# Optimization experiments

Hardware: AMD Instinct MI355X
Metric: run time of the kernel (lower is better)

Reference implementation:

```python
import jax, jax.numpy as jnp
import numpy as np

B, S, D, F, E, K = 2, 1024, 2048, 1024, 8, 2


def setup_inputs() -> dict:
    key = jax.random.key(0)
    ks = jax.random.split(key, 5)
    scale_x = 0.02
    return {
        "x": jax.random.normal(ks[0], (B, S, D), dtype=jnp.float32),
        "w_router": jax.random.normal(ks[1], (E, D), dtype=jnp.float32) * scale_x,
        "w_gate": jax.random.normal(ks[2], (E, F, D), dtype=jnp.float32) * scale_x,
        "w_up": jax.random.normal(ks[3], (E, F, D), dtype=jnp.float32) * scale_x,
        "w_down": jax.random.normal(ks[4], (E, D, F), dtype=jnp.float32) * scale_x,
        "top_k": K,
    }


def reference(x, w_router, w_gate, w_up, w_down, top_k):
    # Router: logits [B,S,E] -> top-k indices + softmax over top-k logits (fp32)
    logits = jnp.einsum("bsd,ed->bse", x, w_router)
    top_logits, top_idx = jax.lax.top_k(logits, top_k)          # [B,S,K]
    gates = jax.nn.softmax(top_logits.astype(jnp.float32), axis=-1)
    # SwitchGLU: per-expert gated MLP. Compute all experts densely, then gather
    # the selected expert output per token (reference-faithful math).
    h = jax.nn.silu(jnp.einsum("bsd,efd->besf", x, w_gate)) * jnp.einsum(
        "bsd,efd->besf", x, w_up
    )                                                            # [B,E,S,F]
    out_all = jnp.einsum("besf,edf->bsed", h, w_down)            # [B,S,E,D]
    y = jnp.take_along_axis(out_all, top_idx[..., None], axis=2)  # [B,S,K,D]
    return (y * gates[..., None].astype(y.dtype)).sum(axis=-2)   # [B,S,D]
```

## Files before the change

kernel.cpp:

```cpp
#include <hip/hip_runtime.h>
#include <hip/hip_bf16.h>

#define T_TOK 2048
#define DIM   2048
#define FFN   1024
#define NE    8

typedef __attribute__((ext_vector_type(8))) short bf16x8;
typedef __attribute__((ext_vector_type(4))) float f32x4;

__device__ __forceinline__ unsigned short f2bf(float f) {
  __hip_bfloat16 h = __float2bfloat16(f);
  return __builtin_bit_cast(unsigned short, h);
}

__device__ __forceinline__ void gload_lds16(const unsigned short* g, unsigned short* l) {
  __builtin_amdgcn_global_load_lds(
      (const __attribute__((address_space(1))) void*)g,
      (__attribute__((address_space(3))) void*)l, 16, 0, 0);
}

__global__ void zero_out(float4* __restrict__ o, int n4) {
  int i = blockIdx.x * blockDim.x + threadIdx.x;
  int stride = gridDim.x * blockDim.x;
  float4 z = {0.f, 0.f, 0.f, 0.f};
  for (; i < n4; i += stride) o[i] = z;
}

__global__ __launch_bounds__(256) void cvt_w(
    const float* __restrict__ wg, const float* __restrict__ wu, const float* __restrict__ wd,
    unsigned short* __restrict__ wgb, unsigned short* __restrict__ wub,
    unsigned short* __restrict__ wdb) {
  int b = blockIdx.x;
  const float* src; unsigned short* dst;
  if (b < 2048)       { src = wg; dst = wgb; }
  else if (b < 4096)  { src = wu; dst = wub; b -= 2048; }
  else                { src = wd; dst = wdb; b -= 4096; }
  const f32x4* s = reinterpret_cast<const f32x4*>(src) + (long)b * 2048 + threadIdx.x;
  ushort4* d = reinterpret_cast<ushort4*>(dst) + (long)b * 2048 + threadIdx.x;
  f32x4 v[8];
#pragma unroll
  for (int g = 0; g < 8; ++g) v[g] = __builtin_nontemporal_load(&s[g * 256]);
#pragma unroll
  for (int g = 0; g < 8; ++g) {
    ushort4 o;
    o.x = f2bf(v[g][0]); o.y = f2bf(v[g][1]); o.z = f2bf(v[g][2]); o.w = f2bf(v[g][3]);
    d[g * 256] = o;
  }
}

__global__ __launch_bounds__(256) void router_topk(
    const float* __restrict__ x, const float* __restrict__ wr,
    int* __restrict__ top_i, float* __restrict__ top_g,
    unsigned short* __restrict__ xb) {
  int t = blockIdx.x * 4 + (threadIdx.x >> 6);
  int lane = threadIdx.x & 63;
  const float4* xr = reinterpret_cast<const float4*>(x) + (size_t)t * (DIM / 4);
  const float4* wrv = reinterpret_cast<const float4*>(wr);
  ushort4* xbr = reinterpret_cast<ushort4*>(xb + (size_t)t * DIM);
  float acc[NE];
#pragma unroll
  for (int e = 0; e < NE; ++e) acc[e] = 0.f;
#pragma unroll
  for (int it = 0; it < DIM / 4 / 64; ++it) {
    int d4 = it * 64 + lane;
    float4 xv = xr[d4];
    ushort4 o;
    o.x = f2bf(xv.x); o.y = f2bf(xv.y); o.z = f2bf(xv.z); o.w = f2bf(xv.w);
    xbr[d4] = o;
#pragma unroll
    for (int e = 0; e < NE; ++e) {
      float4 wv = wrv[e * (DIM / 4) + d4];
      acc[e] += xv.x * wv.x + xv.y * wv.y + xv.z * wv.z + xv.w * wv.w;
    }
  }
#pragma unroll
  for (int off = 32; off > 0; off >>= 1) {
#pragma unroll
    for (int e = 0; e < NE; ++e) acc[e] += __shfl_xor(acc[e], off, 64);
  }
  if (lane == 0) {
    int i0 = 0; float m0 = acc[0];
#pragma unroll
    for (int e = 1; e < NE; ++e) if (acc[e] > m0) { m0 = acc[e]; i0 = e; }
    int i1 = -1; float m1 = -3.4e38f;
#pragma unroll
    for (int e = 0; e < NE; ++e) if (e != i0 && acc[e] > m1) { m1 = acc[e]; i1 = e; }
    float tv = expf(m1 - m0);
    float den = 1.f + tv;
    top_i[t * 2 + 0] = i0; top_i[t * 2 + 1] = i1;
    top_g[t * 2 + 0] = 1.f / den; top_g[t * 2 + 1] = tv / den;
  }
}

__global__ void count_offsets(const int* __restrict__ top_i,
                              int* __restrict__ offs, int* __restrict__ cursor) {
  __shared__ int cnt[NE];
  if (threadIdx.x < NE) cnt[threadIdx.x] = 0;
  __syncthreads();
  for (int i = threadIdx.x; i < T_TOK * 2; i += blockDim.x) atomicAdd(&cnt[top_i[i]], 1);
  __syncthreads();
  if (threadIdx.x == 0) {
    int s = 0;
    for (int e = 0; e < NE; ++e) { offs[e] = s; cursor[e] = s; s += cnt[e]; }
    offs[NE] = s;
  }
}

__global__ void scatter_tokens(const int* __restrict__ top_i, const float* __restrict__ top_g,
                               int* __restrict__ cursor, int* __restrict__ tok_list,
                               float* __restrict__ gate_lst) {
  int t = blockIdx.x * blockDim.x + threadIdx.x;
  if (t >= T_TOK) return;
#pragma unroll
  for (int s = 0; s < 2; ++s) {
    int e = top_i[t * 2 + s];
    int p = atomicAdd(&cursor[e], 1);
    tok_list[p] = t;
    gate_lst[p] = top_g[t * 2 + s];
  }
}

__global__ __launch_bounds__(256, 4) void gateup_gemm(
    const unsigned short* __restrict__ xb, const unsigned short* __restrict__ wgb,
    const unsigned short* __restrict__ wub, const int* __restrict__ tok_list,
    const int* __restrict__ offs, unsigned short* __restrict__ hbuf) {
  const int e = blockIdx.z;
  const int row0 = offs[e];
  const int n_e = offs[e + 1] - row0;
  const int mt = blockIdx.y;
  if (mt * 64 >= n_e) return;
  const int nt = blockIdx.x;

  __shared__ unsigned short As[64 * 64];
  __shared__ unsigned short Bg[64 * 64];
  __shared__ unsigned short Bu[64 * 64];

  const int tid = threadIdx.x;
  const int wid = tid >> 6;
  const int lane = tid & 63;

  const int gchunk = (((lane & 7) ^ ((lane >> 3) & 7)) << 3);

  const unsigned short* gA[2];
  int lAoff[2];
#pragma unroll
  for (int p = 0; p < 2; ++p) {
    int rt = wid * 16 + p * 8 + (lane >> 3);
    int ar = mt * 64 + rt; if (ar >= n_e) ar = n_e - 1;
    gA[p] = xb + (size_t)tok_list[row0 + ar] * DIM + gchunk;
    lAoff[p] = (wid * 16 + p * 8) * 64;
  }
  const size_t wbase = (size_t)e * FFN * DIM + (size_t)(nt * 64) * DIM;
  const unsigned short* gG[2];
  const unsigned short* gU[2];
  int lBoff[2];
#pragma unroll
  for (int p = 0; p < 2; ++p) {
    int rt = wid * 16 + p * 8 + (lane >> 3);
    gG[p] = wgb + wbase + (size_t)rt * DIM + gchunk;
    gU[p] = wub + wbase + (size_t)rt * DIM + gchunk;
    lBoff[p] = (wid * 16 + p * 8) * 64;
  }

  f32x4 accg[2][2];
  f32x4 accu[2][2];
#pragma unroll
  for (int i = 0; i < 2; ++i)
#pragma unroll
    for (int j = 0; j < 2; ++j) {
      accg[i][j] = (f32x4){0.f, 0.f, 0.f, 0.f};
      accu[i][j] = (f32x4){0.f, 0.f, 0.f, 0.f};
    }

  const int warow = (wid >> 1) * 32;
  const int wacol = (wid & 1) * 32;
  const int frow = lane & 15;
  const int eo0 = ((((lane >> 4)) ^ (lane & 7)) << 3);
  const int eo1 = (((4 + (lane >> 4)) ^ (lane & 7)) << 3);

  for (int k0 = 0; k0 < DIM; k0 += 64) {
#pragma unroll
    for (int p = 0; p < 2; ++p) {
      gload_lds16(gA[p] + k0, &As[lAoff[p]]);
      gload_lds16(gG[p] + k0, &Bg[lBoff[p]]);
      gload_lds16(gU[p] + k0, &Bu[lBoff[p]]);
    }
    __syncthreads();
#pragma unroll
    for (int kk = 0; kk < 2; ++kk) {
      const int eo = kk ? eo1 : eo0;
      bf16x8 af[2], bg[2], bu[2];
#pragma unroll
      for (int i = 0; i < 2; ++i)
        af[i] = *reinterpret_cast<const bf16x8*>(&As[(warow + i * 16 + frow) * 64 + eo]);
#pragma unroll
      for (int j = 0; j < 2; ++j) {
        bg[j] = *reinterpret_cast<const bf16x8*>(&Bg[(wacol + j * 16 + frow) * 64 + eo]);
        bu[j] = *reinterpret_cast<const bf16x8*>(&Bu[(wacol + j * 16 + frow) * 64 + eo]);
      }
#pragma unroll
      for (int i = 0; i < 2; ++i)
#pragma unroll
        for (int j = 0; j < 2; ++j) {
          accg[i][j] = __builtin_amdgcn_mfma_f32_16x16x32_bf16(af[i], bg[j], accg[i][j], 0, 0, 0);
          accu[i][j] = __builtin_amdgcn_mfma_f32_16x16x32_bf16(af[i], bu[j], accu[i][j], 0, 0, 0);
        }
    }
    __syncthreads();
  }

#pragma unroll
  for (int i = 0; i < 2; ++i) {
#pragma unroll
    for (int jj = 0; jj < 4; ++jj) {
      int r = mt * 64 + warow + i * 16 + (lane >> 4) * 4 + jj;
      if (r < n_e) {
#pragma unroll
        for (int j = 0; j < 2; ++j) {
          float g = accg[i][j][jj];
          float u = accu[i][j][jj];
          float h = (g / (1.f + __expf(-g))) * u;
          int f = nt * 64 + wacol + j * 16 + (lane & 15);
          hbuf[(size_t)(row0 + r) * FFN + f] = f2bf(h);
        }
      }
    }
  }
}

__global__ __launch_bounds__(256, 4) void down_gemm(
    const unsigned short* __restrict__ hbuf, const unsigned short* __restrict__ wdb,
    const int* __restrict__ tok_list, const float* __restrict__ gate_lst,
    const int* __restrict__ offs, float* __restrict__ out) {
  const int e = blockIdx.z;
  const int row0 = offs[e];
  const int n_e = offs[e + 1] - row0;
  const int mt = blockIdx.y;
  if (mt * 64 >= n_e) return;
  const int nt = blockIdx.x;

  __shared__ unsigned short As[64 * 64];
  __shared__ unsigned short Bs[128 * 64];

  const int tid = threadIdx.x;
  const int wid = tid >> 6;
  const int lane = tid & 63;

  const int gchunk = (((lane & 7) ^ ((lane >> 3) & 7)) << 3);

  const unsigned short* gA[2];
  int lAoff[2];
#pragma unroll
  for (int p = 0; p < 2; ++p) {
    int rt = wid * 16 + p * 8 + (lane >> 3);
    int ar = mt * 64 + rt; if (ar >= n_e) ar = n_e - 1;
    gA[p] = hbuf + (size_t)(row0 + ar) * FFN + gchunk;
    lAoff[p] = (wid * 16 + p * 8) * 64;
  }
  const unsigned short* gB[4];
  int lBoff[4];
#pragma unroll
  for (int p = 0; p < 4; ++p) {
    int rt = wid * 32 + p * 8 + (lane >> 3);
    gB[p] = wdb + ((size_t)e * DIM + nt * 128 + rt) * FFN + gchunk;
    lBoff[p] = (wid * 32 + p * 8) * 64;
  }

  f32x4 acc[2][4];
#pragma unroll
  for (int i = 0; i < 2; ++i)
#pragma unroll
    for (int j = 0; j < 4; ++j) acc[i][j] = (f32x4){0.f, 0.f, 0.f, 0.f};

  const int warow = (wid >> 1) * 32;
  const int wacol = (wid & 1) * 64;
  const int frow = lane & 15;
  const int eo0 = ((((lane >> 4)) ^ (lane & 7)) << 3);
  const int eo1 = (((4 + (lane >> 4)) ^ (lane & 7)) << 3);

  for (int k0 = 0; k0 < FFN; k0 += 64) {
#pragma unroll
    for (int p = 0; p < 2; ++p) gload_lds16(gA[p] + k0, &As[lAoff[p]]);
#pragma unroll
    for (int p = 0; p < 4; ++p) gload_lds16(gB[p] + k0, &Bs[lBoff[p]]);
    __syncthreads();
#pragma unroll
    for (int kk = 0; kk < 2; ++kk) {
      const int eo = kk ? eo1 : eo0;
      bf16x8 af[2], bf[4];
#pragma unroll
      for (int i = 0; i < 2; ++i)
        af[i] = *reinterpret_cast<const bf16x8*>(&As[(warow + i * 16 + frow) * 64 + eo]);
#pragma unroll
      for (int j = 0; j < 4; ++j)
        bf[j] = *reinterpret_cast<const bf16x8*>(&Bs[(wacol + j * 16 + frow) * 64 + eo]);
#pragma unroll
      for (int i = 0; i < 2; ++i)
#pragma unroll
        for (int j = 0; j < 4; ++j)
          acc[i][j] = __builtin_amdgcn_mfma_f32_16x16x32_bf16(af[i], bf[j], acc[i][j], 0, 0, 0);
    }
    __syncthreads();
  }

#pragma unroll
  for (int i = 0; i < 2; ++i) {
#pragma unroll
    for (int jj = 0; jj < 4; ++jj) {
      int r = mt * 64 + warow + i * 16 + (lane >> 4) * 4 + jj;
      if (r < n_e) {
        int tk = tok_list[row0 + r];
        float gt = gate_lst[row0 + r];
        float* yrow = out + (size_t)tk * DIM;
#pragma unroll
        for (int j = 0; j < 4; ++j) {
          int d = nt * 128 + wacol + j * 16 + (lane & 15);
          atomicAdd(&yrow[d], gt * acc[i][j][jj]);
        }
      }
    }
  }
}

extern "C" void kernel_launch(void* const* d_in, const int* in_sizes, int n_in,
                              void* d_out, int out_size, void* d_ws, size_t ws_size,
                              hipStream_t stream) {
  const float* x = (const float*)d_in[0];
  const float* wr = (const float*)d_in[1];
  const float* wg = (const float*)d_in[2];
  const float* wu = (const float*)d_in[3];
  const float* wd = (const float*)d_in[4];
  float* out = (float*)d_out;

  char* ws = (char*)d_ws;
  size_t off = 0;
  auto alloc = [&](size_t bytes) {
    char* p = ws + off;
    off += (bytes + 255) & ~(size_t)255;
    return p;
  };
  unsigned short* xb   = (unsigned short*)alloc((size_t)T_TOK * DIM * 2);
  unsigned short* wgb  = (unsigned short*)alloc((size_t)NE * FFN * DIM * 2);
  unsigned short* wub  = (unsigned short*)alloc((size_t)NE * FFN * DIM * 2);
  unsigned short* wdb  = (unsigned short*)alloc((size_t)NE * DIM * FFN * 2);
  unsigned short* hbuf = (unsigned short*)alloc((size_t)T_TOK * 2 * FFN * 2);
  int* top_i     = (int*)alloc(T_TOK * 2 * 4);
  float* top_g   = (float*)alloc(T_TOK * 2 * 4);
  int* tok_list  = (int*)alloc(T_TOK * 2 * 4);
  float* gate_lst = (float*)alloc(T_TOK * 2 * 4);
  int* offs      = (int*)alloc(64);
  int* cursor    = (int*)alloc(64);
  if (off > ws_size) return;

  zero_out<<<1024, 256, 0, stream>>>((float4*)out, T_TOK * DIM / 4);
  cvt_w<<<6144, 256, 0, stream>>>(wg, wu, wd, wgb, wub, wdb);
  router_topk<<<T_TOK / 4, 256, 0, stream>>>(x, wr, top_i, top_g, xb);
  count_offsets<<<1, 256, 0, stream>>>(top_i, offs, cursor);
  scatter_tokens<<<(T_TOK + 255) / 256, 256, 0, stream>>>(top_i, top_g, cursor, tok_list,
                                                          gate_lst);
  gateup_gemm<<<dim3(FFN / 64, 32, NE), 256, 0, stream>>>(xb, wgb, wub, tok_list, offs, hbuf);
  down_gemm<<<dim3(DIM / 128, 32, NE), 256, 0, stream>>>(hbuf, wdb, tok_list, gate_lst,
                                                         offs, out);
}
```

Before: 201.5 us.

## Double-buffer LDS tiles in gate/up and down expert GEMMs

Both grouped GEMM kernels now keep two LDS buffers per operand and issue the async global-to-LDS loads for the next K tile before the MFMA work on the current tile. This lets memory latency overlap with matrix compute instead of stalling on the barrier after each load. It doubles LDS use per block (about 48 KB in each kernel). Launch bounds drop from 4 to 3 blocks per CU to match, which lowers occupancy in exchange for the overlap.

```diff
diff --git a/kernel.cpp b/kernel.cpp
--- a/kernel.cpp
+++ b/kernel.cpp
@@ -121,7 +121,7 @@
   }
 }
 
-__global__ __launch_bounds__(256, 4) void gateup_gemm(
+__global__ __launch_bounds__(256, 3) void gateup_gemm(
     const unsigned short* __restrict__ xb, const unsigned short* __restrict__ wgb,
     const unsigned short* __restrict__ wub, const int* __restrict__ tok_list,
     const int* __restrict__ offs, unsigned short* __restrict__ hbuf) {
@@ -132,9 +132,9 @@
   if (mt * 64 >= n_e) return;
   const int nt = blockIdx.x;
 
-  __shared__ unsigned short As[64 * 64];
-  __shared__ unsigned short Bg[64 * 64];
-  __shared__ unsigned short Bu[64 * 64];
+  __shared__ unsigned short As[2][64 * 64];
+  __shared__ unsigned short Bg[2][64 * 64];
+  __shared__ unsigned short Bu[2][64 * 64];
 
   const int tid = threadIdx.x;
   const int wid = tid >> 6;
@@ -163,6 +163,15 @@
     lBoff[p] = (wid * 16 + p * 8) * 64;
   }
 
+  auto stage = [&](int buf, int k0) {
+#pragma unroll
+    for (int p = 0; p < 2; ++p) {
+      gload_lds16(gA[p] + k0, &As[buf][lAoff[p]]);
+      gload_lds16(gG[p] + k0, &Bg[buf][lBoff[p]]);
+      gload_lds16(gU[p] + k0, &Bu[buf][lBoff[p]]);
+    }
+  };
+
   f32x4 accg[2][2];
   f32x4 accu[2][2];
 #pragma unroll
@@ -179,25 +188,24 @@
   const int eo0 = ((((lane >> 4)) ^ (lane & 7)) << 3);
   const int eo1 = (((4 + (lane >> 4)) ^ (lane & 7)) << 3);
 
-  for (int k0 = 0; k0 < DIM; k0 += 64) {
-#pragma unroll
-    for (int p = 0; p < 2; ++p) {
-      gload_lds16(gA[p] + k0, &As[lAoff[p]]);
-      gload_lds16(gG[p] + k0, &Bg[lBoff[p]]);
-      gload_lds16(gU[p] + k0, &Bu[lBoff[p]]);
-    }
-    __syncthreads();
+  stage(0, 0);
+  __syncthreads();
+
+  const int NT = DIM / 64;
+  int cur = 0;
+  for (int t = 0; t < NT; ++t) {
+    if (t + 1 < NT) stage(cur ^ 1, (t + 1) * 64);
 #pragma unroll
     for (int kk = 0; kk < 2; ++kk) {
       const int eo = kk ? eo1 : eo0;
       bf16x8 af[2], bg[2], bu[2];
 #pragma unroll
       for (int i = 0; i < 2; ++i)
-        af[i] = *reinterpret_cast<const bf16x8*>(&As[(warow + i * 16 + frow) * 64 + eo]);
+        af[i] = *reinterpret_cast<const bf16x8*>(&As[cur][(warow + i * 16 + frow) * 64 + eo]);
 #pragma unroll
       for (int j = 0; j < 2; ++j) {
-        bg[j] = *reinterpret_cast<const bf16x8*>(&Bg[(wacol + j * 16 + frow) * 64 + eo]);
-        bu[j] = *reinterpret_cast<const bf16x8*>(&Bu[(wacol + j * 16 + frow) * 64 + eo]);
+        bg[j] = *reinterpret_cast<const bf16x8*>(&Bg[cur][(wacol + j * 16 + frow) * 64 + eo]);
+        bu[j] = *reinterpret_cast<const bf16x8*>(&Bu[cur][(wacol + j * 16 + frow) * 64 + eo]);
       }
 #pragma unroll
       for (int i = 0; i < 2; ++i)
@@ -208,6 +216,7 @@
         }
     }
     __syncthreads();
+    cur ^= 1;
   }
 
 #pragma unroll
@@ -229,7 +238,7 @@
   }
 }
 
-__global__ __launch_bounds__(256, 4) void down_gemm(
+__global__ __launch_bounds__(256, 3) void down_gemm(
     const unsigned short* __restrict__ hbuf, const unsigned short* __restrict__ wdb,
     const int* __restrict__ tok_list, const float* __restrict__ gate_lst,
     const int* __restrict__ offs, float* __restrict__ out) {
@@ -240,8 +249,8 @@
   if (mt * 64 >= n_e) return;
   const int nt = blockIdx.x;
 
-  __shared__ unsigned short As[64 * 64];
-  __shared__ unsigned short Bs[128 * 64];
+  __shared__ unsigned short As[2][64 * 64];
+  __shared__ unsigned short Bs[2][128 * 64];
 
   const int tid = threadIdx.x;
   const int wid = tid >> 6;
@@ -267,6 +276,13 @@
     lBoff[p] = (wid * 32 + p * 8) * 64;
   }
 
+  auto stage = [&](int buf, int k0) {
+#pragma unroll
+    for (int p = 0; p < 2; ++p) gload_lds16(gA[p] + k0, &As[buf][lAoff[p]]);
+#pragma unroll
+    for (int p = 0; p < 4; ++p) gload_lds16(gB[p] + k0, &Bs[buf][lBoff[p]]);
+  };
+
   f32x4 acc[2][4];
 #pragma unroll
   for (int i = 0; i < 2; ++i)
@@ -279,22 +295,23 @@
   const int eo0 = ((((lane >> 4)) ^ (lane & 7)) << 3);
   const int eo1 = (((4 + (lane >> 4)) ^ (lane & 7)) << 3);
 
-  for (int k0 = 0; k0 < FFN; k0 += 64) {
-#pragma unroll
-    for (int p = 0; p < 2; ++p) gload_lds16(gA[p] + k0, &As[lAoff[p]]);
-#pragma unroll
-    for (int p = 0; p < 4; ++p) gload_lds16(gB[p] + k0, &Bs[lBoff[p]]);
-    __syncthreads();
+  stage(0, 0);
+  __syncthreads();
+
+  const int NT = FFN / 64;
+  int cur = 0;
+  for (int t = 0; t < NT; ++t) {
+    if (t + 1 < NT) stage(cur ^ 1, (t + 1) * 64);
 #pragma unroll
     for (int kk = 0; kk < 2; ++kk) {
       const int eo = kk ? eo1 : eo0;
       bf16x8 af[2], bf[4];
 #pragma unroll
       for (int i = 0; i < 2; ++i)
-        af[i] = *reinterpret_cast<const bf16x8*>(&As[(warow + i * 16 + frow) * 64 + eo]);
+        af[i] = *reinterpret_cast<const bf16x8*>(&As[cur][(warow + i * 16 + frow) * 64 + eo]);
 #pragma unroll
       for (int j = 0; j < 4; ++j)
-        bf[j] = *reinterpret_cast<const bf16x8*>(&Bs[(wacol + j * 16 + frow) * 64 + eo]);
+        bf[j] = *reinterpret_cast<const bf16x8*>(&Bs[cur][(wacol + j * 16 + frow) * 64 + eo]);
 #pragma unroll
       for (int i = 0; i < 2; ++i)
 #pragma unroll
@@ -302,6 +319,7 @@
           acc[i][j] = __builtin_amdgcn_mfma_f32_16x16x32_bf16(af[i], bf[j], acc[i][j], 0, 0, 0);
     }
     __syncthreads();
+    cur ^= 1;
   }
 
 #pragma unroll
```

New measurement: 209.5 us. 1.04x slower.
